# Kernel tuning notes

Hardware: AMD Instinct MI355X
Metric: run time of the kernel (lower is better)

Reference implementation:

```python
import jax, jax.numpy as jnp
import numpy as np

N_S, N_T, E = 50000, 50000, 600000
D_IN, D_H, D_OUT = 256, 128, 64


def setup_inputs() -> dict:
    key = jax.random.key(0)
    k1, k2, k3, k4, k5, k6 = jax.random.split(key, 6)
    edge_src = jax.random.randint(k1, (E,), 0, N_S, dtype=jnp.int32)
    edge_dst = jax.random.randint(k2, (E,), 0, N_T, dtype=jnp.int32)
    edge_index = jnp.stack([edge_src, edge_dst], axis=0)  # [2, E]
    x_s = jax.random.normal(k3, (N_S, D_IN), dtype=jnp.float32)
    x_t = jax.random.normal(k4, (N_T, D_IN), dtype=jnp.float32)
    W0 = jax.random.normal(k5, (D_IN, D_H), dtype=jnp.float32) * (1.0 / np.sqrt(D_IN))
    W1 = jax.random.normal(k6, (D_H, D_OUT), dtype=jnp.float32) * (1.0 / np.sqrt(D_H))
    return {"edge_index": edge_index, "x_s": x_s, "x_t": x_t, "W0": W0, "W1": W1}


def gcn_conv(x, src, dst, W):
    """PyG GCNConv, bias=False: D^{-1/2}(A+I)D^{-1/2} (x @ W)."""
    N = x.shape[0]
    h = x @ W  # [N, out]
    loops = jnp.arange(N, dtype=src.dtype)
    s = jnp.concatenate([src, loops])  # add self-loops
    d = jnp.concatenate([dst, loops])
    deg = jax.ops.segment_sum(jnp.ones_like(d, dtype=h.dtype), d, num_segments=N)
    dinv = jnp.where(deg > 0, jax.lax.rsqrt(deg), 0.0)
    norm = dinv[s] * dinv[d]  # [E+N]
    return jax.ops.segment_sum(h[s] * norm[:, None], d, num_segments=N)


def reference(edge_index, x_s, x_t, W0, W1):
    n_s = x_s.shape[0]
    src = edge_index[0]
    dst = edge_index[1] + n_s  # targets live in the x_t block
    acts = [jax.nn.relu, lambda v: v]
    Ws = [W0, W1]
    for W, act in zip(Ws, acts):
        x = jnp.concatenate([x_s, x_t], axis=0)
        x = act(gcn_conv(x, src, dst, W))
        x_s, x_t = x[:n_s], x[n_s:]
    return (x_s, x_t)
```

## Files before the change

### kernel.cpp

```cpp
#include <hip/hip_runtime.h>
#include <hip/hip_bf16.h>
#include <cstdint>
#include <cstddef>

typedef unsigned short u16;
typedef unsigned int   u32;
typedef __attribute__((ext_vector_type(8))) short bf16x8;
typedef __attribute__((ext_vector_type(4))) float f32x4;

#define D_IN  256
#define D_H   128
#define D_OUT 64
#define LSTR  72
#define LSTR2 136

__device__ __forceinline__ float bf2f(u16 u){
  union { u32 i; float f; } v; v.i = ((u32)u) << 16; return v.f;
}
__device__ __forceinline__ u16 f2bf(float f){
  union { float f; u32 i; } v; v.f = f;
  u32 r = (v.i + 0x7fffu + ((v.i >> 16) & 1u)) >> 16;
  return (u16)r;
}

__global__ void k_wprep(const float* __restrict__ W0, const float* __restrict__ W1,
                        u16* __restrict__ W0t, u16* __restrict__ W1t,
                        int* __restrict__ deg, int n_t){
  int i = blockIdx.x * 256 + threadIdx.x;
  if (i < 128 * 256){
    int n = i >> 8, k = i & 255;
    W0t[i] = f2bf(W0[(size_t)k * 128 + n]);
  } else if (i < 128 * 256 + 64 * 128){
    int j = i - 128 * 256;
    int n = j >> 7, k = j & 127;
    W1t[j] = f2bf(W1[(size_t)k * 64 + n]);
  } else if (i - (128 * 256 + 64 * 128) < n_t){
    deg[i - (128 * 256 + 64 * 128)] = 0;
  }
}

__global__ void k_deg(const int* __restrict__ dst, int E, int* __restrict__ deg){
  int e = blockIdx.x * 256 + threadIdx.x;
  if (e < E) atomicAdd(&deg[dst[e]], 1);
}

__global__ __launch_bounds__(256) void k_off(const int* __restrict__ deg, int N,
                                             int* __restrict__ off, int* __restrict__ cursor,
                                             float* __restrict__ dinv){
  __shared__ int s[256];
  __shared__ int sbase[256];
  const int tid = threadIdx.x;
  const int bid = blockIdx.x;
  const int i   = bid * 256 + tid;
  const int lim = bid * 256;
  int acc = 0;
  for (int j = tid; j < lim; j += 256) acc += deg[j];
  sbase[tid] = acc;
  int v = (i < N) ? deg[i] : 0;
  s[tid] = v;
  __syncthreads();
  for (int o = 128; o > 0; o >>= 1){
    if (tid < o) sbase[tid] += sbase[tid + o];
    __syncthreads();
  }
  for (int o = 1; o < 256; o <<= 1){
    int t = (tid >= o) ? s[tid - o] : 0;
    __syncthreads();
    s[tid] += t;
    __syncthreads();
  }
  if (i < N){
    int excl = s[tid] - v + sbase[0];
    off[i] = excl;
    cursor[i] = excl;
    dinv[i] = rsqrtf((float)v + 1.0f);
  }
}

__global__ void k_fill(const int* __restrict__ src, const int* __restrict__ dst,
                       int E, int* __restrict__ cursor, int* __restrict__ csr){
  int e = blockIdx.x * 256 + threadIdx.x;
  if (e < E){
    int d = dst[e];
    int p = atomicAdd(&cursor[d], 1);
    csr[p] = src[e];
  }
}

__global__ __launch_bounds__(256) void k_gemm1(
    const float* __restrict__ Xs, const float* __restrict__ Xt,
    const u16* __restrict__ W0t, int M, int n_s,
    u16* __restrict__ out)
{
  __shared__ u16 As[128 * LSTR];
  __shared__ u16 Bs[128 * LSTR];
  const int t    = threadIdx.x;
  const int wave = t >> 6, lane = t & 63;
  const int wm   = (wave >> 1) * 64, wn = (wave & 1) * 64;
  const int lm   = lane & 15, quad = lane >> 4;
  const int row0 = blockIdx.x * 128;

  f32x4 acc[4][4];
  const f32x4 z = {0.f, 0.f, 0.f, 0.f};
  #pragma unroll
  for (int i = 0; i < 4; i++)
    #pragma unroll
    for (int j = 0; j < 4; j++) acc[i][j] = z;

  const int ar = t >> 1;
  const int kh = (t & 1) * 32;
  const int r  = row0 + ar;
  const float* xp = nullptr;
  if (r < M) xp = (r < n_s) ? (Xs + (size_t)r * D_IN) : (Xt + (size_t)(r - n_s) * D_IN);
  const u16* wrow = W0t + (size_t)ar * D_IN + kh;

  float4 a4[8];
  int4   b4[4];
  if (xp){
    #pragma unroll
    for (int j = 0; j < 8; j++) a4[j] = *(const float4*)(xp + kh + j * 4);
  } else {
    float4 zz = make_float4(0,0,0,0);
    #pragma unroll
    for (int j = 0; j < 8; j++) a4[j] = zz;
  }
  #pragma unroll
  for (int j = 0; j < 4; j++) b4[j] = *(const int4*)(wrow + j * 8);

  for (int k0 = 0; k0 < D_IN; k0 += 64){
    __syncthreads();
    {
      union { int4 q[4]; u32 w[16]; } ab;
      #pragma unroll
      for (int j = 0; j < 8; j++){
        __hip_bfloat162 p0 = __float22bfloat162_rn(float2{a4[j].x, a4[j].y});
        __hip_bfloat162 p1 = __float22bfloat162_rn(float2{a4[j].z, a4[j].w});
        ab.w[2*j]   = *(u32*)&p0;
        ab.w[2*j+1] = *(u32*)&p1;
      }
      u16* ap = &As[ar * LSTR + kh];
      *(int4*)(ap +  0) = ab.q[0];
      *(int4*)(ap +  8) = ab.q[1];
      *(int4*)(ap + 16) = ab.q[2];
      *(int4*)(ap + 24) = ab.q[3];
      u16* bp = &Bs[ar * LSTR + kh];
      *(int4*)(bp +  0) = b4[0];
      *(int4*)(bp +  8) = b4[1];
      *(int4*)(bp + 16) = b4[2];
      *(int4*)(bp + 24) = b4[3];
    }
    __syncthreads();

    if (k0 + 64 < D_IN){
      if (xp){
        #pragma unroll
        for (int j = 0; j < 8; j++) a4[j] = *(const float4*)(xp + k0 + 64 + kh + j * 4);
      }
      #pragma unroll
      for (int j = 0; j < 4; j++) b4[j] = *(const int4*)(wrow + k0 + 64 + j * 8);
    }

    #pragma unroll
    for (int kk = 0; kk < 64; kk += 32){
      bf16x8 af[4], bfr[4];
      #pragma unroll
      for (int i = 0; i < 4; i++)
        af[i] = *(const bf16x8*)&As[(wm + i*16 + lm) * LSTR + kk + quad*8];
      #pragma unroll
      for (int i = 0; i < 4; i++)
        bfr[i] = *(const bf16x8*)&Bs[(wn + i*16 + lm) * LSTR + kk + quad*8];
      #pragma unroll
      for (int mi = 0; mi < 4; mi++)
        #pragma unroll
        for (int ni = 0; ni < 4; ni++)
          acc[mi][ni] = __builtin_amdgcn_mfma_f32_16x16x32_bf16(
              af[mi], bfr[ni], acc[mi][ni], 0, 0, 0);
    }
  }

  #pragma unroll
  for (int mi = 0; mi < 4; mi++){
    int rbase = row0 + wm + mi * 16 + quad * 4;
    #pragma unroll
    for (int rr = 0; rr < 4; rr++){
      int m = rbase + rr;
      if (m >= M) continue;
      u16* op = out + (size_t)m * D_H + wn + lm;
      #pragma unroll
      for (int ni = 0; ni < 4; ni++)
        op[ni * 16] = f2bf(acc[mi][ni][rr]);
    }
  }
}

__global__ __launch_bounds__(256) void k_aggf(
    const int* __restrict__ off, const int* __restrict__ deg,
    const int* __restrict__ csr, const float* __restrict__ dinv,
    u16* __restrict__ h1, int n_s, int n_t)
{
  int w    = (blockIdx.x * 256 + threadIdx.x) >> 6;
  int lane = threadIdx.x & 63;
  if (w >= n_t) return;
  const int g = lane >> 4;
  const int c = lane & 15;
  int start = off[w];
  int n     = deg[w];

  float r[8], p[8];
  #pragma unroll
  for (int q = 0; q < 8; q++){ r[q] = 0.f; p[q] = 0.f; }

  int i = 0;
  for (; i + 8 <= n; i += 8){
    int sa = csr[start + i + g];
    int sb = csr[start + i + 4 + g];
    int4 da = *(const int4*)(h1 + (size_t)sa * D_H + c * 8);
    int4 db = *(const int4*)(h1 + (size_t)sb * D_H + c * 8);
    const u16* ha = (const u16*)&da;
    const u16* hb = (const u16*)&db;
    #pragma unroll
    for (int q = 0; q < 8; q++){
      float va = bf2f(ha[q]), vb = bf2f(hb[q]);
      r[q] += va + vb;
      p[q] += fmaxf(va, 0.f) + fmaxf(vb, 0.f);
    }
  }
  for (; i < n; i += 4){
    if (i + g < n){
      int sa = csr[start + i + g];
      int4 da = *(const int4*)(h1 + (size_t)sa * D_H + c * 8);
      const u16* ha = (const u16*)&da;
      #pragma unroll
      for (int q = 0; q < 8; q++){
        float va = bf2f(ha[q]);
        r[q] += va;
        p[q] += fmaxf(va, 0.f);
      }
    }
  }

  #pragma unroll
  for (int q = 0; q < 8; q++){
    r[q] += __shfl_xor(r[q], 16, 64);
    r[q] += __shfl_xor(r[q], 32, 64);
    p[q] += __shfl_xor(p[q], 16, 64);
    p[q] += __shfl_xor(p[q], 32, 64);
  }

  if (g == 0){
    float di  = dinv[w];
    float di2 = di * di;
    u16* selfp = h1 + (size_t)(n_s + w) * D_H + c * 8;
    int4 hs = *(const int4*)selfp;
    const u16* hh = (const u16*)&hs;
    u16 ob[8];
    #pragma unroll
    for (int q = 0; q < 8; q++){
      float zq = fmaxf(di * r[q] + di2 * bf2f(hh[q]), 0.f);
      float uq = di * p[q] + di2 * zq;
      ob[q] = f2bf(uq);
    }
    *(int4*)selfp = *(int4*)ob;
  }
}

__global__ __launch_bounds__(256) void k_gemm2(
    const u16* __restrict__ h1, const u16* __restrict__ W1t,
    int M, int n_s, float* __restrict__ out)
{
  __shared__ u16 As[128 * LSTR2];
  __shared__ u16 Bs[64 * LSTR2];
  const int t    = threadIdx.x;
  const int wave = t >> 6, lane = t & 63;
  const int wm   = wave * 32;
  const int lm   = lane & 15, quad = lane >> 4;
  const int row0 = blockIdx.x * 128;

  const int ar = t >> 1;
  const int kh = (t & 1) * 64;
  const int r  = row0 + ar;
  const bool relu_a = (r < n_s);
  const int bn = t >> 2;
  const int bk = (t & 3) * 32;

  {
    int4 a4[8];
    if (r < M){
      const u16* hp = h1 + (size_t)r * D_H + kh;
      #pragma unroll
      for (int j = 0; j < 8; j++) a4[j] = *(const int4*)(hp + j * 8);
    } else {
      int4 zz = make_int4(0,0,0,0);
      #pragma unroll
      for (int j = 0; j < 8; j++) a4[j] = zz;
    }
    int4 w4[4];
    const u16* wp = W1t + (size_t)bn * D_H + bk;
    #pragma unroll
    for (int j = 0; j < 4; j++) w4[j] = *(const int4*)(wp + j * 8);

    u16* ap = &As[ar * LSTR2 + kh];
    #pragma unroll
    for (int j = 0; j < 8; j++){
      u16* hh = (u16*)&a4[j];
      if (relu_a){
        #pragma unroll
        for (int q = 0; q < 8; q++)
          hh[q] = (hh[q] & 0x8000u) ? (u16)0 : hh[q];
      }
      *(int4*)(ap + j * 8) = a4[j];
    }
    u16* bp = &Bs[bn * LSTR2 + bk];
    #pragma unroll
    for (int j = 0; j < 4; j++) *(int4*)(bp + j * 8) = w4[j];
  }
  __syncthreads();

  f32x4 acc[2][4];
  const f32x4 z = {0.f, 0.f, 0.f, 0.f};
  #pragma unroll
  for (int i = 0; i < 2; i++)
    #pragma unroll
    for (int j = 0; j < 4; j++) acc[i][j] = z;

  #pragma unroll
  for (int kk = 0; kk < 128; kk += 32){
    bf16x8 af[2], bfr[4];
    #pragma unroll
    for (int i = 0; i < 2; i++)
      af[i] = *(const bf16x8*)&As[(wm + i*16 + lm) * LSTR2 + kk + quad*8];
    #pragma unroll
    for (int i = 0; i < 4; i++)
      bfr[i] = *(const bf16x8*)&Bs[(i*16 + lm) * LSTR2 + kk + quad*8];
    #pragma unroll
    for (int mi = 0; mi < 2; mi++)
      #pragma unroll
      for (int ni = 0; ni < 4; ni++)
        acc[mi][ni] = __builtin_amdgcn_mfma_f32_16x16x32_bf16(
            af[mi], bfr[ni], acc[mi][ni], 0, 0, 0);
  }

  #pragma unroll
  for (int mi = 0; mi < 2; mi++){
    int rbase = row0 + wm + mi * 16 + quad * 4;
    #pragma unroll
    for (int rr = 0; rr < 4; rr++){
      int m = rbase + rr;
      if (m >= M) continue;
      float* op = out + (size_t)m * D_OUT + lm;
      #pragma unroll
      for (int ni = 0; ni < 4; ni++)
        op[ni * 16] = acc[mi][ni][rr];
    }
  }
}

static inline size_t alup(size_t x){ return (x + 255) & ~(size_t)255; }

extern "C" void kernel_launch(void* const* d_in, const int* in_sizes, int n_in,
                              void* d_out, int out_size, void* d_ws, size_t ws_size,
                              hipStream_t stream)
{
  const int*   ei = (const int*)d_in[0];
  const float* xs = (const float*)d_in[1];
  const float* xt = (const float*)d_in[2];
  const float* W0 = (const float*)d_in[3];
  const float* W1 = (const float*)d_in[4];
  const int E   = in_sizes[0] / 2;
  const int n_s = in_sizes[1] / D_IN;
  const int n_t = in_sizes[2] / D_IN;
  const int M   = n_s + n_t;
  const int* src = ei;
  const int* dst = ei + E;
  const int nb_t = (n_t + 255) / 256;

  char* p = (char*)d_ws;
  int*   deg    = (int*)p;    p += alup((size_t)n_t * 4);
  int*   off    = (int*)p;    p += alup((size_t)n_t * 4);
  int*   cursor = (int*)p;    p += alup((size_t)n_t * 4);
  float* dinv   = (float*)p;  p += alup((size_t)n_t * 4);
  int*   csr    = (int*)p;    p += alup((size_t)E * 4);
  u16*   W0t    = (u16*)p;    p += alup((size_t)D_H * D_IN * 2);
  u16*   W1t    = (u16*)p;    p += alup((size_t)D_OUT * D_H * 2);
  u16*   h1     = (u16*)p;    p += alup((size_t)M * D_H * 2);

  const int wprep_n = 128*256 + 64*128 + n_t;
  k_wprep <<<(wprep_n + 255) / 256, 256, 0, stream>>>(W0, W1, W0t, W1t, deg, n_t);
  k_deg   <<<(E + 255) / 256, 256, 0, stream>>>(dst, E, deg);
  k_off   <<<nb_t, 256, 0, stream>>>(deg, n_t, off, cursor, dinv);
  k_fill  <<<(E + 255) / 256, 256, 0, stream>>>(src, dst, E, cursor, csr);

  k_gemm1<<<(M + 127) / 128, 256, 0, stream>>>(xs, xt, W0t, M, n_s, h1);
  k_aggf <<<(n_t + 3) / 4, 256, 0, stream>>>(off, deg, csr, dinv, h1, n_s, n_t);
  k_gemm2<<<(M + 127) / 128, 256, 0, stream>>>(h1, W1t, M, n_s, (float*)d_out);
}
```

Baseline: 298.3 us.

## Load GEMM operands directly from global into MFMA fragments, dropping LDS staging

Both dense GEMM kernels stop staging A and B tiles in shared memory. Each wave now loads its MFMA fragments straight from global memory, relying on L1/L2 for reuse, and all barriers are removed. gemm2 also has each wave compute a 64-row tile, so a block covers 256 rows and the grid halves. This removes LDS traffic and synchronisation, but the same row data is fetched redundantly across waves and the loads are uncoalesced, so performance depends on cache hit rates.

Result: no change. 300.4 us (+0.7%).

```diff
diff --git a/kernel.cpp b/kernel.cpp
--- a/kernel.cpp
+++ b/kernel.cpp
@@ -11,8 +11,6 @@
 #define D_IN  256
 #define D_H   128
 #define D_OUT 64
-#define LSTR  72
-#define LSTR2 136
 
 __device__ __forceinline__ float bf2f(u16 u){
   union { u32 i; float f; } v; v.i = ((u32)u) << 16; return v.f;
@@ -87,19 +85,29 @@
   }
 }
 
-__global__ __launch_bounds__(256) void k_gemm1(
+__global__ __launch_bounds__(256, 3) void k_gemm1(
     const float* __restrict__ Xs, const float* __restrict__ Xt,
     const u16* __restrict__ W0t, int M, int n_s,
     u16* __restrict__ out)
 {
-  __shared__ u16 As[128 * LSTR];
-  __shared__ u16 Bs[128 * LSTR];
   const int t    = threadIdx.x;
   const int wave = t >> 6, lane = t & 63;
   const int wm   = (wave >> 1) * 64, wn = (wave & 1) * 64;
   const int lm   = lane & 15, quad = lane >> 4;
   const int row0 = blockIdx.x * 128;
 
+  const float* xrow[4];
+  #pragma unroll
+  for (int mi = 0; mi < 4; mi++){
+    int r = row0 + wm + mi * 16 + lm;
+    if (r >= M) r = M - 1;
+    xrow[mi] = (r < n_s) ? (Xs + (size_t)r * D_IN) : (Xt + (size_t)(r - n_s) * D_IN);
+  }
+  const u16* brow[4];
+  #pragma unroll
+  for (int ni = 0; ni < 4; ni++)
+    brow[ni] = W0t + (size_t)(wn + ni * 16 + lm) * D_IN;
+
   f32x4 acc[4][4];
   const f32x4 z = {0.f, 0.f, 0.f, 0.f};
   #pragma unroll
@@ -107,75 +115,32 @@
     #pragma unroll
     for (int j = 0; j < 4; j++) acc[i][j] = z;
 
-  const int ar = t >> 1;
-  const int kh = (t & 1) * 32;
-  const int r  = row0 + ar;
-  const float* xp = nullptr;
-  if (r < M) xp = (r < n_s) ? (Xs + (size_t)r * D_IN) : (Xt + (size_t)(r - n_s) * D_IN);
-  const u16* wrow = W0t + (size_t)ar * D_IN + kh;
-
-  float4 a4[8];
-  int4   b4[4];
-  if (xp){
-    #pragma unroll
-    for (int j = 0; j < 8; j++) a4[j] = *(const float4*)(xp + kh + j * 4);
-  } else {
-    float4 zz = make_float4(0,0,0,0);
-    #pragma unroll
-    for (int j = 0; j < 8; j++) a4[j] = zz;
-  }
-  #pragma unroll
-  for (int j = 0; j < 4; j++) b4[j] = *(const int4*)(wrow + j * 8);
-
-  for (int k0 = 0; k0 < D_IN; k0 += 64){
-    __syncthreads();
-    {
-      union { int4 q[4]; u32 w[16]; } ab;
-      #pragma unroll
-      for (int j = 0; j < 8; j++){
-        __hip_bfloat162 p0 = __float22bfloat162_rn(float2{a4[j].x, a4[j].y});
-        __hip_bfloat162 p1 = __float22bfloat162_rn(float2{a4[j].z, a4[j].w});
-        ab.w[2*j]   = *(u32*)&p0;
-        ab.w[2*j+1] = *(u32*)&p1;
-      }
-      u16* ap = &As[ar * LSTR + kh];
-      *(int4*)(ap +  0) = ab.q[0];
-      *(int4*)(ap +  8) = ab.q[1];
-      *(int4*)(ap + 16) = ab.q[2];
-      *(int4*)(ap + 24) = ab.q[3];
-      u16* bp = &Bs[ar * LSTR + kh];
-      *(int4*)(bp +  0) = b4[0];
-      *(int4*)(bp +  8) = b4[1];
-      *(int4*)(bp + 16) = b4[2];
-      *(int4*)(bp + 24) = b4[3];
-    }
-    __syncthreads();
-
-    if (k0 + 64 < D_IN){
-      if (xp){
-        #pragma unroll
-        for (int j = 0; j < 8; j++) a4[j] = *(const float4*)(xp + k0 + 64 + kh + j * 4);
-      }
-      #pragma unroll
-      for (int j = 0; j < 4; j++) b4[j] = *(const int4*)(wrow + k0 + 64 + j * 8);
-    }
-
-    #pragma unroll
-    for (int kk = 0; kk < 64; kk += 32){
-      bf16x8 af[4], bfr[4];
-      #pragma unroll
-      for (int i = 0; i < 4; i++)
-        af[i] = *(const bf16x8*)&As[(wm + i*16 + lm) * LSTR + kk + quad*8];
-      #pragma unroll
-      for (int i = 0; i < 4; i++)
-        bfr[i] = *(const bf16x8*)&Bs[(wn + i*16 + lm) * LSTR + kk + quad*8];
-      #pragma unroll
-      for (int mi = 0; mi < 4; mi++)
-        #pragma unroll
-        for (int ni = 0; ni < 4; ni++)
-          acc[mi][ni] = __builtin_amdgcn_mfma_f32_16x16x32_bf16(
-              af[mi], bfr[ni], acc[mi][ni], 0, 0, 0);
-    }
+  #pragma unroll
+  for (int kc = 0; kc < 8; kc++){
+    const int kk = kc * 32 + quad * 8;
+    bf16x8 af[4], bfr[4];
+    #pragma unroll
+    for (int mi = 0; mi < 4; mi++){
+      float4 lo = *(const float4*)(xrow[mi] + kk);
+      float4 hi = *(const float4*)(xrow[mi] + kk + 4);
+      union { bf16x8 v; u32 w[4]; } u;
+      __hip_bfloat162 p0 = __float22bfloat162_rn(float2{lo.x, lo.y});
+      __hip_bfloat162 p1 = __float22bfloat162_rn(float2{lo.z, lo.w});
+      __hip_bfloat162 p2 = __float22bfloat162_rn(float2{hi.x, hi.y});
+      __hip_bfloat162 p3 = __float22bfloat162_rn(float2{hi.z, hi.w});
+      u.w[0] = *(u32*)&p0; u.w[1] = *(u32*)&p1;
+      u.w[2] = *(u32*)&p2; u.w[3] = *(u32*)&p3;
+      af[mi] = u.v;
+    }
+    #pragma unroll
+    for (int ni = 0; ni < 4; ni++)
+      bfr[ni] = *(const bf16x8*)(brow[ni] + kk);
+    #pragma unroll
+    for (int mi = 0; mi < 4; mi++)
+      #pragma unroll
+      for (int ni = 0; ni < 4; ni++)
+        acc[mi][ni] = __builtin_amdgcn_mfma_f32_16x16x32_bf16(
+            af[mi], bfr[ni], acc[mi][ni], 0, 0, 0);
   }
 
   #pragma unroll
@@ -264,76 +229,56 @@
   }
 }
 
-__global__ __launch_bounds__(256) void k_gemm2(
+__global__ __launch_bounds__(256, 3) void k_gemm2(
     const u16* __restrict__ h1, const u16* __restrict__ W1t,
     int M, int n_s, float* __restrict__ out)
 {
-  __shared__ u16 As[128 * LSTR2];
-  __shared__ u16 Bs[64 * LSTR2];
   const int t    = threadIdx.x;
   const int wave = t >> 6, lane = t & 63;
-  const int wm   = wave * 32;
   const int lm   = lane & 15, quad = lane >> 4;
-  const int row0 = blockIdx.x * 128;
-
-  const int ar = t >> 1;
-  const int kh = (t & 1) * 64;
-  const int r  = row0 + ar;
-  const bool relu_a = (r < n_s);
-  const int bn = t >> 2;
-  const int bk = (t & 3) * 32;
-
-  {
-    int4 a4[8];
-    if (r < M){
-      const u16* hp = h1 + (size_t)r * D_H + kh;
-      #pragma unroll
-      for (int j = 0; j < 8; j++) a4[j] = *(const int4*)(hp + j * 8);
-    } else {
-      int4 zz = make_int4(0,0,0,0);
-      #pragma unroll
-      for (int j = 0; j < 8; j++) a4[j] = zz;
-    }
-    int4 w4[4];
-    const u16* wp = W1t + (size_t)bn * D_H + bk;
-    #pragma unroll
-    for (int j = 0; j < 4; j++) w4[j] = *(const int4*)(wp + j * 8);
-
-    u16* ap = &As[ar * LSTR2 + kh];
-    #pragma unroll
-    for (int j = 0; j < 8; j++){
-      u16* hh = (u16*)&a4[j];
-      if (relu_a){
+  const int rowbase = blockIdx.x * 256 + wave * 64;
+
+  const u16* arow[4];
+  bool relu[4];
+  #pragma unroll
+  for (int mi = 0; mi < 4; mi++){
+    int r = rowbase + mi * 16 + lm;
+    if (r >= M) r = M - 1;
+    relu[mi] = (r < n_s);
+    arow[mi] = h1 + (size_t)r * D_H;
+  }
+  const u16* brow[4];
+  #pragma unroll
+  for (int ni = 0; ni < 4; ni++)
+    brow[ni] = W1t + (size_t)(ni * 16 + lm) * D_H;
+
+  f32x4 acc[4][4];
+  const f32x4 z = {0.f, 0.f, 0.f, 0.f};
+  #pragma unroll
+  for (int i = 0; i < 4; i++)
+    #pragma unroll
+    for (int j = 0; j < 4; j++) acc[i][j] = z;
+
+  #pragma unroll
+  for (int kc = 0; kc < 4; kc++){
+    const int kk = kc * 32 + quad * 8;
+    bf16x8 af[4], bfr[4];
+    #pragma unroll
+    for (int mi = 0; mi < 4; mi++){
+      union { int4 q; u16 h[8]; } u;
+      u.q = *(const int4*)(arow[mi] + kk);
+      if (relu[mi]){
         #pragma unroll
-        for (int q = 0; q < 8; q++)
-          hh[q] = (hh[q] & 0x8000u) ? (u16)0 : hh[q];
+        for (int qq = 0; qq < 8; qq++)
+          u.h[qq] = (u.h[qq] & 0x8000u) ? (u16)0 : u.h[qq];
       }
-      *(int4*)(ap + j * 8) = a4[j];
-    }
-    u16* bp = &Bs[bn * LSTR2 + bk];
-    #pragma unroll
-    for (int j = 0; j < 4; j++) *(int4*)(bp + j * 8) = w4[j];
-  }
-  __syncthreads();
-
-  f32x4 acc[2][4];
-  const f32x4 z = {0.f, 0.f, 0.f, 0.f};
-  #pragma unroll
-  for (int i = 0; i < 2; i++)
-    #pragma unroll
-    for (int j = 0; j < 4; j++) acc[i][j] = z;
-
-  #pragma unroll
-  for (int kk = 0; kk < 128; kk += 32){
-    bf16x8 af[2], bfr[4];
-    #pragma unroll
-    for (int i = 0; i < 2; i++)
-      af[i] = *(const bf16x8*)&As[(wm + i*16 + lm) * LSTR2 + kk + quad*8];
-    #pragma unroll
-    for (int i = 0; i < 4; i++)
-      bfr[i] = *(const bf16x8*)&Bs[(i*16 + lm) * LSTR2 + kk + quad*8];
-    #pragma unroll
-    for (int mi = 0; mi < 2; mi++)
+      af[mi] = *(bf16x8*)&u.q;
+    }
+    #pragma unroll
+    for (int ni = 0; ni < 4; ni++)
+      bfr[ni] = *(const bf16x8*)(brow[ni] + kk);
+    #pragma unroll
+    for (int mi = 0; mi < 4; mi++)
       #pragma unroll
       for (int ni = 0; ni < 4; ni++)
         acc[mi][ni] = __builtin_amdgcn_mfma_f32_16x16x32_bf16(
@@ -341,8 +286,8 @@
   }
 
   #pragma unroll
-  for (int mi = 0; mi < 2; mi++){
-    int rbase = row0 + wm + mi * 16 + quad * 4;
+  for (int mi = 0; mi < 4; mi++){
+    int rbase = rowbase + mi * 16 + quad * 4;
     #pragma unroll
     for (int rr = 0; rr < 4; rr++){
       int m = rbase + rr;
@@ -392,5 +337,5 @@
 
   k_gemm1<<<(M + 127) / 128, 256, 0, stream>>>(xs, xt, W0t, M, n_s, h1);
   k_aggf <<<(n_t + 3) / 4, 256, 0, stream>>>(off, deg, csr, dinv, h1, n_s, n_t);
-  k_gemm2<<<(M + 127) / 128, 256, 0, stream>>>(h1, W1t, M, n_s, (float*)d_out);
-}
+  k_gemm2<<<(M + 255) / 256, 256, 0, stream>>>(h1, W1t, M, n_s, (float*)d_out);
+}
```
